# Kernel tuning notes

Hardware: AMD Instinct MI355X
Metric: run time of the kernel (lower is better)

## Reference

```python
import jax, jax.numpy as jnp
import numpy as np

N_NODES = 100000
N_EDGES = 600000
VOCAB = 5000
NUM_GRAPHS = 2000
NUM_CLASSES = 10


def setup_inputs() -> dict:
    key = jax.random.key(0)
    ks = jax.random.split(key, 12)
    x = jax.random.randint(ks[0], (N_NODES,), 0, VOCAB, dtype=jnp.int32)
    edge_index = jax.random.randint(ks[1], (2, N_EDGES), 0, N_NODES, dtype=jnp.int32)
    batch = jnp.sort(jax.random.randint(ks[2], (N_NODES,), 0, NUM_GRAPHS, dtype=jnp.int32))
    emb = jax.random.normal(ks[3], (VOCAB, 64), dtype=jnp.float32) * 0.1
    W1 = jax.random.normal(ks[4], (64, 128), dtype=jnp.float32) * (1.0 / np.sqrt(64))
    b1 = jnp.zeros((128,), dtype=jnp.float32)
    W2 = jax.random.normal(ks[5], (128, 128), dtype=jnp.float32) * (1.0 / np.sqrt(128))
    b2 = jnp.zeros((128,), dtype=jnp.float32)
    Wlin = jax.random.normal(ks[6], (128, NUM_CLASSES), dtype=jnp.float32) * (1.0 / np.sqrt(128))
    blin = jnp.zeros((NUM_CLASSES,), dtype=jnp.float32)
    return {"x": x, "edge_index": edge_index, "batch": batch, "num_graphs": NUM_GRAPHS,
            "emb": emb, "W1": W1, "b1": b1, "W2": W2, "b2": b2, "Wlin": Wlin, "blin": blin}


def reference(x, edge_index, batch, num_graphs, emb, W1, b1, W2, b2, Wlin, blin):
    N = x.shape[0]
    loops = jnp.arange(N, dtype=edge_index.dtype)
    src = jnp.concatenate([edge_index[0], loops])  # message sources (j)
    dst = jnp.concatenate([edge_index[1], loops])  # aggregation targets (i)
    # GCN symmetric normalization with self-loops (PyG gcn_norm, source_to_target)
    deg = jax.ops.segment_sum(jnp.ones_like(dst, dtype=jnp.float32), dst, num_segments=N)
    dinv = jnp.where(deg > 0, jax.lax.rsqrt(deg), 0.0)
    norm = dinv[src] * dinv[dst]  # [E+N]

    def gcn(h, W, b):
        h = h @ W  # linear transform first (GCNConv order)
        msg = h[src] * norm[:, None]  # gather + scale, [E+N, F]
        return jax.ops.segment_sum(msg, dst, num_segments=N) + b

    h = emb[x]  # [N, 64]
    h = jax.nn.relu(gcn(h, W1, b1))
    h = jax.nn.relu(gcn(h, W2, b2))
    g = jax.ops.segment_max(h, batch, num_segments=num_graphs)  # global_max_pool
    return g @ Wlin + blin
```

## Files before the change

### kernel.cpp

```cpp
#include <hip/hip_runtime.h>
#include <hip/hip_bf16.h>
#include <hip/hip_fp16.h>


typedef _Float16 h4v __attribute__((ext_vector_type(4)));
typedef _Float16 h8 __attribute__((ext_vector_type(8)));
typedef float f32x4 __attribute__((ext_vector_type(4)));

__global__ __launch_bounds__(256) void k_degprep(const int* __restrict__ dst, int* __restrict__ deg, int E,
                                                 const float* __restrict__ emb, const float* __restrict__ W1,
                                                 __half2* __restrict__ T, const float* __restrict__ W2,
                                                 _Float16* __restrict__ W2T, int VOCAB, int gE, int nEmb) {
    int bid = blockIdx.x;
    if (bid < gE) {
        int e = bid * 256 + threadIdx.x;
        if (e < E) atomicAdd(&deg[dst[e]], 1);
    } else if (bid < gE + nEmb) {
        int t = (bid - gE) * 256 + threadIdx.x;
        if (t >= VOCAB * 32) return;
        int v = t >> 5, cq = t & 31;
        const float* er = emb + (size_t)v * 64;
        float4 acc = make_float4(0.f, 0.f, 0.f, 0.f);
#pragma unroll 8
        for (int k = 0; k < 64; ++k) {
            float e = er[k];
            float4 w = *(const float4*)&W1[k * 128 + cq * 4];
            acc.x += e * w.x; acc.y += e * w.y; acc.z += e * w.z; acc.w += e * w.w;
        }
        __half2* o = T + (size_t)v * 64 + cq * 2;
        o[0] = __floats2half2_rn(acc.x, acc.y);
        o[1] = __floats2half2_rn(acc.z, acc.w);
    } else {
        int t = (bid - gE - nEmb) * 256 + threadIdx.x;
        if (t >= 128 * 128) return;
        int c = t >> 7, k = t & 127;
        W2T[c * 128 + k] = (_Float16)W2[k * 128 + c];
    }
}

__global__ __launch_bounds__(256) void k_scan1(const int* __restrict__ deg, int* __restrict__ exc,
                                               int* __restrict__ bsums, float* __restrict__ dinv, int N) {
    __shared__ int s[256];
    int i = blockIdx.x * 256 + threadIdx.x;
    int v = (i < N) ? deg[i] : 0;
    if (i < N) dinv[i] = rsqrtf((float)(v + 1));
    s[threadIdx.x] = v;
    __syncthreads();
    for (int off = 1; off < 256; off <<= 1) {
        int t = (threadIdx.x >= (unsigned)off) ? s[threadIdx.x - off] : 0;
        __syncthreads();
        s[threadIdx.x] += t;
        __syncthreads();
    }
    if (i < N) exc[i] = s[threadIdx.x] - v;
    if (threadIdx.x == 255) bsums[blockIdx.x] = s[255];
}

__global__ __launch_bounds__(512) void k_scan2(int* __restrict__ bsums, int nb) {
    __shared__ int s[512];
    int i = threadIdx.x;
    int v = (i < nb) ? bsums[i] : 0;
    s[i] = v;
    __syncthreads();
    for (int off = 1; off < 512; off <<= 1) {
        int t = (i >= off) ? s[i - off] : 0;
        __syncthreads();
        s[i] += t;
        __syncthreads();
    }
    if (i < nb) bsums[i] = s[i] - v;
}

__global__ __launch_bounds__(256) void k_scan3(int* __restrict__ rowstart, int* __restrict__ cursor,
                                               const int* __restrict__ bsums, int N, int E) {
    int i = blockIdx.x * 256 + threadIdx.x;
    if (i < N) {
        int r = rowstart[i] + bsums[blockIdx.x];
        rowstart[i] = r;
        cursor[i] = r;
    }
    if (i == 0 && blockIdx.x == 0) rowstart[N] = E;
}

__global__ __launch_bounds__(256) void k_fill(const int* __restrict__ src, const int* __restrict__ dst,
                                              const int* __restrict__ x, const float* __restrict__ dinv,
                                              int* __restrict__ cursor, int4* __restrict__ rec, int E) {
    int e = blockIdx.x * 256 + threadIdx.x;
    if (e < E) {
        int d = dst[e];
        int s = src[e];
        int pos = atomicAdd(&cursor[d], 1);
        rec[pos] = make_int4(x[s], __float_as_int(dinv[s]), s, 0);
    }
}

__global__ __launch_bounds__(256) void k_agg1(const h4v* __restrict__ T4, const int* __restrict__ x,
                                              const float* __restrict__ dinv, const int* __restrict__ rs,
                                              const int4* __restrict__ rec, const float4* __restrict__ bias4,
                                              h4v* __restrict__ h1, int N) {
    int lane = threadIdx.x & 31;
    int n0 = (blockIdx.x * 8 + (threadIdx.x >> 5)) * 2;
    if (n0 >= N) return;
    int nB = (n0 + 1 < N) ? n0 + 1 : n0;
    int cA0 = rs[n0], cA1 = rs[n0 + 1];
    int cB0 = rs[nB], cB1 = rs[nB + 1];
    bool hasA = cA0 < cA1, hasB = cB0 < cB1;
    h4v tA[8], tB[8];
    float wA[8], wB[8];
    if (hasA) {
#pragma unroll
        for (int i = 0; i < 8; ++i) {
            int ei = cA0 + i;
            int ec = (ei < cA1) ? ei : cA1 - 1;
            int4 r = rec[ec];
            tA[i] = T4[(size_t)r.x * 32 + lane];
            wA[i] = (ei < cA1) ? __int_as_float(r.y) : 0.f;
        }
    }
    if (hasB) {
#pragma unroll
        for (int i = 0; i < 8; ++i) {
            int ei = cB0 + i;
            int ec = (ei < cB1) ? ei : cB1 - 1;
            int4 r = rec[ec];
            tB[i] = T4[(size_t)r.x * 32 + lane];
            wB[i] = (ei < cB1) ? __int_as_float(r.y) : 0.f;
        }
    }
    float dA = dinv[n0], dB = dinv[nB];
    h4v sA = T4[(size_t)x[n0] * 32 + lane];
    h4v sB = T4[(size_t)x[nB] * 32 + lane];
    float aA[4], aB[4];
#pragma unroll
    for (int f = 0; f < 4; ++f) {
        aA[f] = dA * (float)sA[f];
        aB[f] = dB * (float)sB[f];
    }
    if (hasA) {
#pragma unroll
        for (int i = 0; i < 8; ++i)
#pragma unroll
            for (int f = 0; f < 4; ++f) aA[f] = fmaf(wA[i], (float)tA[i][f], aA[f]);
    }
    if (hasB) {
#pragma unroll
        for (int i = 0; i < 8; ++i)
#pragma unroll
            for (int f = 0; f < 4; ++f) aB[f] = fmaf(wB[i], (float)tB[i][f], aB[f]);
    }
    for (int e = cA0 + 8; e < cA1; e += 8) {
#pragma unroll
        for (int i = 0; i < 8; ++i) {
            int ei = e + i;
            int ec = (ei < cA1) ? ei : cA1 - 1;
            int4 r = rec[ec];
            tA[i] = T4[(size_t)r.x * 32 + lane];
            wA[i] = (ei < cA1) ? __int_as_float(r.y) : 0.f;
        }
#pragma unroll
        for (int i = 0; i < 8; ++i)
#pragma unroll
            for (int f = 0; f < 4; ++f) aA[f] = fmaf(wA[i], (float)tA[i][f], aA[f]);
    }
    for (int e = cB0 + 8; e < cB1; e += 8) {
#pragma unroll
        for (int i = 0; i < 8; ++i) {
            int ei = e + i;
            int ec = (ei < cB1) ? ei : cB1 - 1;
            int4 r = rec[ec];
            tB[i] = T4[(size_t)r.x * 32 + lane];
            wB[i] = (ei < cB1) ? __int_as_float(r.y) : 0.f;
        }
#pragma unroll
        for (int i = 0; i < 8; ++i)
#pragma unroll
            for (int f = 0; f < 4; ++f) aB[f] = fmaf(wB[i], (float)tB[i][f], aB[f]);
    }
    float4 b = bias4[lane];
    float bv[4] = {b.x, b.y, b.z, b.w};
    h4v oA, oB;
#pragma unroll
    for (int f = 0; f < 4; ++f) {
        oA[f] = (_Float16)fmaxf(fmaf(dA, aA[f], bv[f]), 0.f);
        oB[f] = (_Float16)fmaxf(fmaf(dB, aB[f], bv[f]), 0.f);
    }
    h1[(size_t)n0 * 32 + lane] = oA;
    h1[(size_t)nB * 32 + lane] = oB;
}

__global__ __launch_bounds__(256) void k_gemm(const _Float16* __restrict__ A, const _Float16* __restrict__ W2T,
                                              const float* __restrict__ dinv, _Float16* __restrict__ P, int N) {
    int lane = threadIdx.x & 63;
    int wid = threadIdx.x >> 6;
    int r = lane & 15, kg = lane >> 4;
    int row0 = blockIdx.x * 64 + wid * 16;
    int arow = row0 + r;
    if (arow >= N) arow = N - 1;
    const _Float16* ab = A + (size_t)arow * 128 + kg * 8;
    const _Float16* bb = W2T + (size_t)r * 128 + kg * 8;
    f32x4 acc[8];
#pragma unroll
    for (int ct = 0; ct < 8; ++ct) acc[ct] = (f32x4){0.f, 0.f, 0.f, 0.f};
#pragma unroll
    for (int kc = 0; kc < 4; ++kc) {
        h8 a = *(const h8*)(ab + kc * 32);
#pragma unroll
        for (int ct = 0; ct < 8; ++ct) {
            h8 b = *(const h8*)(bb + kc * 32 + ct * 2048);
            acc[ct] = __builtin_amdgcn_mfma_f32_16x16x32_f16(a, b, acc[ct], 0, 0, 0);
        }
    }
    float dv[4];
#pragma unroll
    for (int i = 0; i < 4; ++i) {
        int gr = row0 + 4 * kg + i;
        dv[i] = (gr < N) ? dinv[gr] : 0.f;
    }
#pragma unroll
    for (int ct = 0; ct < 8; ++ct) {
#pragma unroll
        for (int i = 0; i < 4; ++i) {
            int gr = row0 + 4 * kg + i;
            if (gr < N) P[(size_t)gr * 128 + ct * 16 + r] = (_Float16)(acc[ct][i] * dv[i]);
        }
    }
}

__global__ __launch_bounds__(512) void k_agg2pool(const h4v* __restrict__ P4, const int* __restrict__ batch,
                                                  const float* __restrict__ dinv, const int* __restrict__ rs,
                                                  const int4* __restrict__ rec, const float4* __restrict__ bias4,
                                                  float* __restrict__ pool, int N, int G) {
    __shared__ int lpool[4][128];
    int tid = threadIdx.x;
    lpool[tid >> 7][tid & 127] = 0;
    __syncthreads();
    int lane = tid & 31;
    int blk_n0 = blockIdx.x * 32;
    int gfirst = batch[(blk_n0 < N) ? blk_n0 : (N - 1)];
    int n0 = blk_n0 + (tid >> 5) * 2;
    if (n0 < N) {
        int nB = (n0 + 1 < N) ? n0 + 1 : n0;
        int cA0 = rs[n0], cA1 = rs[n0 + 1];
        int cB0 = rs[nB], cB1 = rs[nB + 1];
        bool hasA = cA0 < cA1, hasB = cB0 < cB1;
        h4v tA[8], tB[8];
        float wA[8], wB[8];
        if (hasA) {
#pragma unroll
            for (int i = 0; i < 8; ++i) {
                int ei = cA0 + i;
                int ec = (ei < cA1) ? ei : cA1 - 1;
                tA[i] = P4[(size_t)rec[ec].z * 32 + lane];
                wA[i] = (ei < cA1) ? 1.f : 0.f;
            }
        }
        if (hasB) {
#pragma unroll
            for (int i = 0; i < 8; ++i) {
                int ei = cB0 + i;
                int ec = (ei < cB1) ? ei : cB1 - 1;
                tB[i] = P4[(size_t)rec[ec].z * 32 + lane];
                wB[i] = (ei < cB1) ? 1.f : 0.f;
            }
        }
        h4v sA = P4[(size_t)n0 * 32 + lane];
        h4v sB = P4[(size_t)nB * 32 + lane];
        float aA[4], aB[4];
#pragma unroll
        for (int f = 0; f < 4; ++f) {
            aA[f] = (float)sA[f];
            aB[f] = (float)sB[f];
        }
        if (hasA) {
#pragma unroll
            for (int i = 0; i < 8; ++i)
#pragma unroll
                for (int f = 0; f < 4; ++f) aA[f] = fmaf(wA[i], (float)tA[i][f], aA[f]);
        }
        if (hasB) {
#pragma unroll
            for (int i = 0; i < 8; ++i)
#pragma unroll
                for (int f = 0; f < 4; ++f) aB[f] = fmaf(wB[i], (float)tB[i][f], aB[f]);
        }
        for (int e = cA0 + 8; e < cA1; e += 8) {
#pragma unroll
            for (int i = 0; i < 8; ++i) {
                int ei = e + i;
                int ec = (ei < cA1) ? ei : cA1 - 1;
                tA[i] = P4[(size_t)rec[ec].z * 32 + lane];
                wA[i] = (ei < cA1) ? 1.f : 0.f;
            }
#pragma unroll
            for (int i = 0; i < 8; ++i)
#pragma unroll
                for (int f = 0; f < 4; ++f) aA[f] = fmaf(wA[i], (float)tA[i][f], aA[f]);
        }
        for (int e = cB0 + 8; e < cB1; e += 8) {
#pragma unroll
            for (int i = 0; i < 8; ++i) {
                int ei = e + i;
                int ec = (ei < cB1) ? ei : cB1 - 1;
                tB[i] = P4[(size_t)rec[ec].z * 32 + lane];
                wB[i] = (ei < cB1) ? 1.f : 0.f;
            }
#pragma unroll
            for (int i = 0; i < 8; ++i)
#pragma unroll
                for (int f = 0; f < 4; ++f) aB[f] = fmaf(wB[i], (float)tB[i][f], aB[f]);
        }
        float dA = dinv[n0], dB = dinv[nB];
        int gA = batch[n0], gB = batch[nB];
        float4 b = bias4[lane];
        float bv[4] = {b.x, b.y, b.z, b.w};
        float zA[4], zB[4];
#pragma unroll
        for (int f = 0; f < 4; ++f) {
            zA[f] = fmaxf(fmaf(dA, aA[f], bv[f]), 0.f);
            zB[f] = fmaxf(fmaf(dB, aB[f], bv[f]), 0.f);
        }
        auto emit = [&](int g, const float* m) {
            int slot = g - gfirst;
            if (slot < 4) {
#pragma unroll
                for (int f = 0; f < 4; ++f)
                    if (m[f] > 0.f) atomicMax(&lpool[slot][lane * 4 + f], __float_as_int(m[f]));
            } else {
                float* pg = pool + (size_t)g * 128 + lane * 4;
#pragma unroll
                for (int f = 0; f < 4; ++f)
                    if (m[f] > 0.f) atomicMax((int*)(pg + f), __float_as_int(m[f]));
            }
        };
        if (gA == gB) {
            float m[4];
#pragma unroll
            for (int f = 0; f < 4; ++f) m[f] = fmaxf(zA[f], zB[f]);
            emit(gA, m);
        } else {
            emit(gA, zA);
            emit(gB, zB);
        }
    }
    __syncthreads();
    int s = tid >> 7, f = tid & 127;
    int v = lpool[s][f];
    if (v > 0) atomicMax((int*)&pool[(size_t)(gfirst + s) * 128 + f], v);
}

__global__ __launch_bounds__(256) void k_final(const float* __restrict__ pool, const float* __restrict__ Wlin,
                                               const float* __restrict__ blin, float* __restrict__ out, int G) {
    int t = blockIdx.x * 256 + threadIdx.x;
    if (t >= G * 10) return;
    int g = t / 10, c = t % 10;
    float acc = blin[c];
    const float* pr = pool + (size_t)g * 128;
#pragma unroll 8
    for (int f = 0; f < 128; ++f) acc = fmaf(pr[f], Wlin[f * 10 + c], acc);
    out[t] = acc;
}

extern "C" void kernel_launch(void* const* d_in, const int* in_sizes, int n_in,
                              void* d_out, int out_size, void* d_ws, size_t ws_size,
                              hipStream_t stream) {
    const int* x = (const int*)d_in[0];
    const int* ei = (const int*)d_in[1];
    const int* batch = (const int*)d_in[2];
    const float* emb = (const float*)d_in[4];
    const float* W1 = (const float*)d_in[5];
    const float* b1 = (const float*)d_in[6];
    const float* W2 = (const float*)d_in[7];
    const float* b2 = (const float*)d_in[8];
    const float* Wlin = (const float*)d_in[9];
    const float* blin = (const float*)d_in[10];
    float* out = (float*)d_out;

    int N = in_sizes[0];
    int E = in_sizes[1] / 2;
    int VOCAB = in_sizes[4] / 64;
    int G = out_size / 10;
    const int* srcp = ei;
    const int* dstp = ei + E;

    char* p = (char*)d_ws;
    auto alloc = [&](size_t bytes) -> char* {
        char* r = p;
        p += (bytes + 255) & ~(size_t)255;
        return r;
    };
    int* deg = (int*)alloc((size_t)N * 4);
    int* cursor = (int*)alloc((size_t)N * 4);
    int* rowstart = (int*)alloc((size_t)(N + 1) * 4);
    int* bsums = (int*)alloc(512 * 4);
    float* dinv = (float*)alloc((size_t)N * 4);
    int4* rec = (int4*)alloc((size_t)E * 16);
    _Float16* T = (_Float16*)alloc((size_t)VOCAB * 128 * 2);
    _Float16* W2T = (_Float16*)alloc(128 * 128 * 2);
    _Float16* h1 = (_Float16*)alloc((size_t)N * 128 * 2);
    _Float16* P = (_Float16*)alloc((size_t)N * 128 * 2);
    float* pool = (float*)alloc((size_t)G * 128 * 4);

    hipMemsetAsync(deg, 0, (size_t)N * 4, stream);
    hipMemsetAsync(pool, 0, (size_t)G * 128 * 4, stream);

    int gE = (E + 255) / 256;
    int gN = (N + 255) / 256;
    int nEmb = (VOCAB * 32 + 255) / 256;

    k_degprep<<<gE + nEmb + 64, 256, 0, stream>>>(dstp, deg, E, emb, W1, (__half2*)T, W2, W2T,
                                                  VOCAB, gE, nEmb);
    k_scan1<<<gN, 256, 0, stream>>>(deg, rowstart, bsums, dinv, N);
    k_scan2<<<1, 512, 0, stream>>>(bsums, gN);
    k_scan3<<<gN, 256, 0, stream>>>(rowstart, cursor, bsums, N, E);
    k_fill<<<gE, 256, 0, stream>>>(srcp, dstp, x, dinv, cursor, rec, E);
    k_agg1<<<(N + 15) / 16, 256, 0, stream>>>((const h4v*)T, x, dinv, rowstart, rec,
                                              (const float4*)b1, (h4v*)h1, N);
    k_gemm<<<(N + 63) / 64, 256, 0, stream>>>(h1, W2T, dinv, P, N);
    k_agg2pool<<<(N + 31) / 32, 512, 0, stream>>>((const h4v*)P, batch, dinv, rowstart, rec,
                                                  (const float4*)b2, pool, N, G);
    k_final<<<(G * 10 + 255) / 256, 256, 0, stream>>>(pool, Wlin, blin, out, G);
}
```

Baseline: 209.1 us.

## Aggregate 64-wide embeddings before layer-1 GEMM and split edge records

```diff
diff --git a/kernel.cpp b/kernel.cpp
--- a/kernel.cpp
+++ b/kernel.cpp
@@ -3,38 +3,43 @@
 #include <hip/hip_fp16.h>
 
 
-typedef _Float16 h4v __attribute__((ext_vector_type(4)));
 typedef _Float16 h8 __attribute__((ext_vector_type(8)));
 typedef float f32x4 __attribute__((ext_vector_type(4)));
 
+__global__ __launch_bounds__(256) void k_zero(int4* __restrict__ deg, int n4i,
+                                              int4* __restrict__ pool, int p4i) {
+    int t = blockIdx.x * 256 + threadIdx.x;
+    int4 z = make_int4(0, 0, 0, 0);
+    if (t < n4i) deg[t] = z;
+    if (t < p4i) pool[t] = z;
+}
+
 __global__ __launch_bounds__(256) void k_degprep(const int* __restrict__ dst, int* __restrict__ deg, int E,
-                                                 const float* __restrict__ emb, const float* __restrict__ W1,
-                                                 __half2* __restrict__ T, const float* __restrict__ W2,
-                                                 _Float16* __restrict__ W2T, int VOCAB, int gE, int nEmb) {
+                                                 const float* __restrict__ emb, __half2* __restrict__ e16,
+                                                 const float* __restrict__ W1, _Float16* __restrict__ W1T,
+                                                 const float* __restrict__ W2, _Float16* __restrict__ W2T,
+                                                 int nEmbF, int gE, int nCast) {
     int bid = blockIdx.x;
     if (bid < gE) {
         int e = bid * 256 + threadIdx.x;
         if (e < E) atomicAdd(&deg[dst[e]], 1);
-    } else if (bid < gE + nEmb) {
+    } else if (bid < gE + nCast) {
         int t = (bid - gE) * 256 + threadIdx.x;
-        if (t >= VOCAB * 32) return;
-        int v = t >> 5, cq = t & 31;
-        const float* er = emb + (size_t)v * 64;
-        float4 acc = make_float4(0.f, 0.f, 0.f, 0.f);
-#pragma unroll 8
-        for (int k = 0; k < 64; ++k) {
-            float e = er[k];
-            float4 w = *(const float4*)&W1[k * 128 + cq * 4];
-            acc.x += e * w.x; acc.y += e * w.y; acc.z += e * w.z; acc.w += e * w.w;
-        }
-        __half2* o = T + (size_t)v * 64 + cq * 2;
-        o[0] = __floats2half2_rn(acc.x, acc.y);
-        o[1] = __floats2half2_rn(acc.z, acc.w);
+        if (t * 4 < nEmbF) {
+            float4 v = *(const float4*)&emb[t * 4];
+            e16[t * 2] = __floats2half2_rn(v.x, v.y);
+            e16[t * 2 + 1] = __floats2half2_rn(v.z, v.w);
+        }
+    } else if (bid < gE + nCast + 32) {
+        int t = (bid - gE - nCast) * 256 + threadIdx.x;
+        int c = t >> 6, k = t & 63;
+        W1T[c * 64 + k] = (_Float16)W1[k * 128 + c];
     } else {
-        int t = (bid - gE - nEmb) * 256 + threadIdx.x;
-        if (t >= 128 * 128) return;
-        int c = t >> 7, k = t & 127;
-        W2T[c * 128 + k] = (_Float16)W2[k * 128 + c];
+        int t = (bid - gE - nCast - 32) * 256 + threadIdx.x;
+        if (t < 128 * 128) {
+            int c = t >> 7, k = t & 127;
+            W2T[c * 128 + k] = (_Float16)W2[k * 128 + c];
+        }
     }
 }
 
@@ -84,20 +89,21 @@
 
 __global__ __launch_bounds__(256) void k_fill(const int* __restrict__ src, const int* __restrict__ dst,
                                               const int* __restrict__ x, const float* __restrict__ dinv,
-                                              int* __restrict__ cursor, int4* __restrict__ rec, int E) {
+                                              int* __restrict__ cursor, int2* __restrict__ ed,
+                                              int* __restrict__ cols, int E) {
     int e = blockIdx.x * 256 + threadIdx.x;
     if (e < E) {
         int d = dst[e];
         int s = src[e];
         int pos = atomicAdd(&cursor[d], 1);
-        rec[pos] = make_int4(x[s], __float_as_int(dinv[s]), s, 0);
-    }
-}
-
-__global__ __launch_bounds__(256) void k_agg1(const h4v* __restrict__ T4, const int* __restrict__ x,
+        ed[pos] = make_int2(x[s], __float_as_int(dinv[s]));
+        cols[pos] = s;
+    }
+}
+
+__global__ __launch_bounds__(256) void k_agge(const __half2* __restrict__ e16, const int* __restrict__ x,
                                               const float* __restrict__ dinv, const int* __restrict__ rs,
-                                              const int4* __restrict__ rec, const float4* __restrict__ bias4,
-                                              h4v* __restrict__ h1, int N) {
+                                              const int2* __restrict__ ed, __half2* __restrict__ Xagg, int N) {
     int lane = threadIdx.x & 31;
     int n0 = (blockIdx.x * 8 + (threadIdx.x >> 5)) * 2;
     if (n0 >= N) return;
@@ -105,15 +111,15 @@
     int cA0 = rs[n0], cA1 = rs[n0 + 1];
     int cB0 = rs[nB], cB1 = rs[nB + 1];
     bool hasA = cA0 < cA1, hasB = cB0 < cB1;
-    h4v tA[8], tB[8];
+    __half2 tA[8], tB[8];
     float wA[8], wB[8];
     if (hasA) {
 #pragma unroll
         for (int i = 0; i < 8; ++i) {
             int ei = cA0 + i;
             int ec = (ei < cA1) ? ei : cA1 - 1;
-            int4 r = rec[ec];
-            tA[i] = T4[(size_t)r.x * 32 + lane];
+            int2 r = ed[ec];
+            tA[i] = e16[(size_t)r.x * 32 + lane];
             wA[i] = (ei < cA1) ? __int_as_float(r.y) : 0.f;
         }
     }
@@ -122,74 +128,104 @@
         for (int i = 0; i < 8; ++i) {
             int ei = cB0 + i;
             int ec = (ei < cB1) ? ei : cB1 - 1;
-            int4 r = rec[ec];
-            tB[i] = T4[(size_t)r.x * 32 + lane];
+            int2 r = ed[ec];
+            tB[i] = e16[(size_t)r.x * 32 + lane];
             wB[i] = (ei < cB1) ? __int_as_float(r.y) : 0.f;
         }
     }
     float dA = dinv[n0], dB = dinv[nB];
-    h4v sA = T4[(size_t)x[n0] * 32 + lane];
-    h4v sB = T4[(size_t)x[nB] * 32 + lane];
-    float aA[4], aB[4];
-#pragma unroll
-    for (int f = 0; f < 4; ++f) {
-        aA[f] = dA * (float)sA[f];
-        aB[f] = dB * (float)sB[f];
-    }
+    float2 sA = __half22float2(e16[(size_t)x[n0] * 32 + lane]);
+    float2 sB = __half22float2(e16[(size_t)x[nB] * 32 + lane]);
+    float aA0 = dA * sA.x, aA1 = dA * sA.y;
+    float aB0 = dB * sB.x, aB1 = dB * sB.y;
     if (hasA) {
 #pragma unroll
-        for (int i = 0; i < 8; ++i)
-#pragma unroll
-            for (int f = 0; f < 4; ++f) aA[f] = fmaf(wA[i], (float)tA[i][f], aA[f]);
+        for (int i = 0; i < 8; ++i) {
+            float2 tf = __half22float2(tA[i]);
+            aA0 = fmaf(wA[i], tf.x, aA0);
+            aA1 = fmaf(wA[i], tf.y, aA1);
+        }
     }
     if (hasB) {
 #pragma unroll
-        for (int i = 0; i < 8; ++i)
-#pragma unroll
-            for (int f = 0; f < 4; ++f) aB[f] = fmaf(wB[i], (float)tB[i][f], aB[f]);
+        for (int i = 0; i < 8; ++i) {
+            float2 tf = __half22float2(tB[i]);
+            aB0 = fmaf(wB[i], tf.x, aB0);
+            aB1 = fmaf(wB[i], tf.y, aB1);
+        }
     }
     for (int e = cA0 + 8; e < cA1; e += 8) {
 #pragma unroll
         for (int i = 0; i < 8; ++i) {
             int ei = e + i;
             int ec = (ei < cA1) ? ei : cA1 - 1;
-            int4 r = rec[ec];
-            tA[i] = T4[(size_t)r.x * 32 + lane];
+            int2 r = ed[ec];
+            tA[i] = e16[(size_t)r.x * 32 + lane];
             wA[i] = (ei < cA1) ? __int_as_float(r.y) : 0.f;
         }
 #pragma unroll
-        for (int i = 0; i < 8; ++i)
-#pragma unroll
-            for (int f = 0; f < 4; ++f) aA[f] = fmaf(wA[i], (float)tA[i][f], aA[f]);
+        for (int i = 0; i < 8; ++i) {
+            float2 tf = __half22float2(tA[i]);
+            aA0 = fmaf(wA[i], tf.x, aA0);
+            aA1 = fmaf(wA[i], tf.y, aA1);
+        }
     }
     for (int e = cB0 + 8; e < cB1; e += 8) {
 #pragma unroll
         for (int i = 0; i < 8; ++i) {
             int ei = e + i;
             int ec = (ei < cB1) ? ei : cB1 - 1;
-            int4 r = rec[ec];
-            tB[i] = T4[(size_t)r.x * 32 + lane];
+            int2 r = ed[ec];
+            tB[i] = e16[(size_t)r.x * 32 + lane];
             wB[i] = (ei < cB1) ? __int_as_float(r.y) : 0.f;
         }
 #pragma unroll
-        for (int i = 0; i < 8; ++i)
-#pragma unroll
-            for (int f = 0; f < 4; ++f) aB[f] = fmaf(wB[i], (float)tB[i][f], aB[f]);
-    }
-    float4 b = bias4[lane];
-    float bv[4] = {b.x, b.y, b.z, b.w};
-    h4v oA, oB;
-#pragma unroll
-    for (int f = 0; f < 4; ++f) {
-        oA[f] = (_Float16)fmaxf(fmaf(dA, aA[f], bv[f]), 0.f);
-        oB[f] = (_Float16)fmaxf(fmaf(dB, aB[f], bv[f]), 0.f);
-    }
-    h1[(size_t)n0 * 32 + lane] = oA;
-    h1[(size_t)nB * 32 + lane] = oB;
-}
-
-__global__ __launch_bounds__(256) void k_gemm(const _Float16* __restrict__ A, const _Float16* __restrict__ W2T,
-                                              const float* __restrict__ dinv, _Float16* __restrict__ P, int N) {
+        for (int i = 0; i < 8; ++i) {
+            float2 tf = __half22float2(tB[i]);
+            aB0 = fmaf(wB[i], tf.x, aB0);
+            aB1 = fmaf(wB[i], tf.y, aB1);
+        }
+    }
+    Xagg[(size_t)n0 * 32 + lane] = __floats2half2_rn(dA * aA0, dA * aA1);
+    Xagg[(size_t)nB * 32 + lane] = __floats2half2_rn(dB * aB0, dB * aB1);
+}
+
+__global__ __launch_bounds__(256) void k_gemm1(const _Float16* __restrict__ A, const _Float16* __restrict__ W1T,
+                                               const float* __restrict__ b1, _Float16* __restrict__ h1, int N) {
+    int lane = threadIdx.x & 63;
+    int wid = threadIdx.x >> 6;
+    int r = lane & 15, kg = lane >> 4;
+    int row0 = blockIdx.x * 64 + wid * 16;
+    int arow = row0 + r;
+    if (arow >= N) arow = N - 1;
+    const _Float16* ab = A + (size_t)arow * 64 + kg * 8;
+    const _Float16* bb = W1T + (size_t)r * 64 + kg * 8;
+    f32x4 acc[8];
+#pragma unroll
+    for (int ct = 0; ct < 8; ++ct) acc[ct] = (f32x4){0.f, 0.f, 0.f, 0.f};
+#pragma unroll
+    for (int kc = 0; kc < 2; ++kc) {
+        h8 a = *(const h8*)(ab + kc * 32);
+#pragma unroll
+        for (int ct = 0; ct < 8; ++ct) {
+            h8 b = *(const h8*)(bb + kc * 32 + ct * 1024);
+            acc[ct] = __builtin_amdgcn_mfma_f32_16x16x32_f16(a, b, acc[ct], 0, 0, 0);
+        }
+    }
+#pragma unroll
+    for (int ct = 0; ct < 8; ++ct) {
+        float bias = b1[ct * 16 + r];
+#pragma unroll
+        for (int i = 0; i < 4; ++i) {
+            int gr = row0 + 4 * kg + i;
+            if (gr < N)
+                h1[(size_t)gr * 128 + ct * 16 + r] = (_Float16)fmaxf(acc[ct][i] + bias, 0.f);
+        }
+    }
+}
+
+__global__ __launch_bounds__(256) void k_gemm2(const _Float16* __restrict__ A, const _Float16* __restrict__ W2T,
+                                               const float* __restrict__ dinv, _Float16* __restrict__ P, int N) {
     int lane = threadIdx.x & 63;
     int wid = threadIdx.x >> 6;
     int r = lane & 15, kg = lane >> 4;
@@ -226,9 +262,11 @@
     }
 }
 
+typedef _Float16 h4v __attribute__((ext_vector_type(4)));
+
 __global__ __launch_bounds__(512) void k_agg2pool(const h4v* __restrict__ P4, const int* __restrict__ batch,
                                                   const float* __restrict__ dinv, const int* __restrict__ rs,
-                                                  const int4* __restrict__ rec, const float4* __restrict__ bias4,
+                                                  const int* __restrict__ cols, const float4* __restrict__ bias4,
                                                   float* __restrict__ pool, int N, int G) {
     __shared__ int lpool[4][128];
     int tid = threadIdx.x;
@@ -250,7 +288,7 @@
             for (int i = 0; i < 8; ++i) {
                 int ei = cA0 + i;
                 int ec = (ei < cA1) ? ei : cA1 - 1;
-                tA[i] = P4[(size_t)rec[ec].z * 32 + lane];
+                tA[i] = P4[(size_t)cols[ec] * 32 + lane];
                 wA[i] = (ei < cA1) ? 1.f : 0.f;
             }
         }
@@ -259,7 +297,7 @@
             for (int i = 0; i < 8; ++i) {
                 int ei = cB0 + i;
                 int ec = (ei < cB1) ? ei : cB1 - 1;
-                tB[i] = P4[(size_t)rec[ec].z * 32 + lane];
+                tB[i] = P4[(size_t)cols[ec] * 32 + lane];
                 wB[i] = (ei < cB1) ? 1.f : 0.f;
             }
         }
@@ -288,7 +326,7 @@
             for (int i = 0; i < 8; ++i) {
                 int ei = e + i;
                 int ec = (ei < cA1) ? ei : cA1 - 1;
-                tA[i] = P4[(size_t)rec[ec].z * 32 + lane];
+                tA[i] = P4[(size_t)cols[ec] * 32 + lane];
                 wA[i] = (ei < cA1) ? 1.f : 0.f;
             }
 #pragma unroll
@@ -301,7 +339,7 @@
             for (int i = 0; i < 8; ++i) {
                 int ei = e + i;
                 int ec = (ei < cB1) ? ei : cB1 - 1;
-                tB[i] = P4[(size_t)rec[ec].z * 32 + lane];
+                tB[i] = P4[(size_t)cols[ec] * 32 + lane];
                 wB[i] = (ei < cB1) ? 1.f : 0.f;
             }
 #pragma unroll
@@ -319,12 +357,15 @@
             zA[f] = fmaxf(fmaf(dA, aA[f], bv[f]), 0.f);
             zB[f] = fmaxf(fmaf(dB, aB[f], bv[f]), 0.f);
         }
+        int rot = (lane >> 3) & 3;
         auto emit = [&](int g, const float* m) {
             int slot = g - gfirst;
             if (slot < 4) {
 #pragma unroll
-                for (int f = 0; f < 4; ++f)
-                    if (m[f] > 0.f) atomicMax(&lpool[slot][lane * 4 + f], __float_as_int(m[f]));
+                for (int f = 0; f < 4; ++f) {
+                    int ff = (f + rot) & 3;
+                    if (m[ff] > 0.f) atomicMax(&lpool[slot][lane * 4 + ff], __float_as_int(m[ff]));
+                }
             } else {
                 float* pg = pool + (size_t)g * 128 + lane * 4;
 #pragma unroll
@@ -393,30 +434,35 @@
     int* rowstart = (int*)alloc((size_t)(N + 1) * 4);
     int* bsums = (int*)alloc(512 * 4);
     float* dinv = (float*)alloc((size_t)N * 4);
-    int4* rec = (int4*)alloc((size_t)E * 16);
-    _Float16* T = (_Float16*)alloc((size_t)VOCAB * 128 * 2);
+    int2* ed = (int2*)alloc((size_t)E * 8);
+    int* cols = (int*)alloc((size_t)E * 4);
+    _Float16* e16 = (_Float16*)alloc((size_t)VOCAB * 64 * 2);
+    _Float16* W1T = (_Float16*)alloc(128 * 64 * 2);
     _Float16* W2T = (_Float16*)alloc(128 * 128 * 2);
+    _Float16* Xagg = (_Float16*)alloc((size_t)N * 64 * 2);
     _Float16* h1 = (_Float16*)alloc((size_t)N * 128 * 2);
     _Float16* P = (_Float16*)alloc((size_t)N * 128 * 2);
     float* pool = (float*)alloc((size_t)G * 128 * 4);
 
-    hipMemsetAsync(deg, 0, (size_t)N * 4, stream);
-    hipMemsetAsync(pool, 0, (size_t)G * 128 * 4, stream);
-
     int gE = (E + 255) / 256;
     int gN = (N + 255) / 256;
-    int nEmb = (VOCAB * 32 + 255) / 256;
-
-    k_degprep<<<gE + nEmb + 64, 256, 0, stream>>>(dstp, deg, E, emb, W1, (__half2*)T, W2, W2T,
-                                                  VOCAB, gE, nEmb);
+    int nEmbF = VOCAB * 64;
+    int nCast = (nEmbF / 4 + 255) / 256;
+
+    int n4i = N / 4, p4i = G * 128 / 4;
+    int zg = ((n4i > p4i ? n4i : p4i) + 255) / 256;
+    k_zero<<<zg, 256, 0, stream>>>((int4*)deg, n4i, (int4*)pool, p4i);
+    k_degprep<<<gE + nCast + 32 + 64, 256, 0, stream>>>(dstp, deg, E, emb, (__half2*)e16, W1, W1T,
+                                                        W2, W2T, nEmbF, gE, nCast);
     k_scan1<<<gN, 256, 0, stream>>>(deg, rowstart, bsums, dinv, N);
     k_scan2<<<1, 512, 0, stream>>>(bsums, gN);
     k_scan3<<<gN, 256, 0, stream>>>(rowstart, cursor, bsums, N, E);
-    k_fill<<<gE, 256, 0, stream>>>(srcp, dstp, x, dinv, cursor, rec, E);
-    k_agg1<<<(N + 15) / 16, 256, 0, stream>>>((const h4v*)T, x, dinv, rowstart, rec,
-                                              (const float4*)b1, (h4v*)h1, N);
-    k_gemm<<<(N + 63) / 64, 256, 0, stream>>>(h1, W2T, dinv, P, N);
-    k_agg2pool<<<(N + 31) / 32, 512, 0, stream>>>((const h4v*)P, batch, dinv, rowstart, rec,
+    k_fill<<<gE, 256, 0, stream>>>(srcp, dstp, x, dinv, cursor, ed, cols, E);
+    k_agge<<<(N + 15) / 16, 256, 0, stream>>>((const __half2*)e16, x, dinv, rowstart, ed,
+                                              (__half2*)Xagg, N);
+    k_gemm1<<<(N + 63) / 64, 256, 0, stream>>>(Xagg, W1T, b1, h1, N);
+    k_gemm2<<<(N + 63) / 64, 256, 0, stream>>>(h1, W2T, dinv, P, N);
+    k_agg2pool<<<(N + 31) / 32, 512, 0, stream>>>((const h4v*)P, batch, dinv, rowstart, cols,
                                                   (const float4*)b2, pool, N, G);
     k_final<<<(G * 10 + 255) / 256, 256, 0, stream>>>(pool, Wlin, blin, out, G);
 }
```

After: 214.0 us. 1.02x slower.
